# Kernel tuning notes

Measured on AMD Instinct MI355X. Metric: run time of the kernel, lower is better.

Reference implementation:

```python
import jax, jax.numpy as jnp
import numpy as np


def setup_inputs() -> dict:
    key = jax.random.key(0)
    k1, k2, k3 = jax.random.split(key, 3)
    B, K, NPC, D = 64, 1000, 256, 768
    querys = jax.random.normal(k1, (B, D), dtype=jnp.float32)
    data = jax.random.normal(k2, (K, NPC, D), dtype=jnp.float32)      # clustered doc embeddings
    centers = jax.random.normal(k3, (K, D), dtype=jnp.float32)        # cluster centroids
    clusted_idx = jnp.arange(K * NPC, dtype=jnp.int32).reshape(K, NPC)  # global doc id per slot
    return {
        'querys': querys,
        'data': data,
        'centers': centers,
        'clusted_idx': clusted_idx,
        'k': 16,
        'num_search': 10,
    }


def reference(querys, data, centers, clusted_idx, k, num_search):
    """Clustered (IVF-style) cosine top-k search.
    querys: (B,D); data: (K,NPC,D); centers: (K,D); clusted_idx: (K,NPC)
    returns ret_idx (B,k) int, ret_emb (B,k,D) float.
    dist_fn = -cos_sim, so argmin dist == argmax cosine.
    """
    B, D = querys.shape
    eps = jnp.float32(1e-12)
    qn = querys / jnp.maximum(jnp.linalg.norm(querys, axis=1, keepdims=True), eps)
    cn = centers / jnp.maximum(jnp.linalg.norm(centers, axis=1, keepdims=True), eps)

    # ---- first(): pick num_search closest clusters by cosine ----
    cos_c = qn @ cn.T                              # (B, K)
    _, c_idx = jax.lax.top_k(cos_c, num_search)    # (B, S) smallest -cos == largest cos

    # ---- second(): exact cosine search inside selected clusters ----
    cand = data[c_idx]                             # (B, S, NPC, D) gather
    cand_ids = clusted_idx[c_idx]                  # (B, S, NPC)
    cand_norm = jnp.maximum(jnp.linalg.norm(cand, axis=-1), eps)  # (B, S, NPC)
    cos = jnp.einsum('bd,bsnd->bsn', qn, cand) / cand_norm        # (B, S, NPC)

    # ---- merge: global top-k over all candidates ----
    cos_flat = cos.reshape(B, -1)                  # (B, S*NPC)
    _, top = jax.lax.top_k(cos_flat, k)            # (B, k)
    ret_idx = jnp.take_along_axis(cand_ids.reshape(B, -1), top, axis=1)            # (B, k)
    ret_emb = jnp.take_along_axis(cand.reshape(B, -1, D), top[..., None], axis=1)  # (B, k, D)
    return ret_idx, ret_emb
```

## Files before the change

kernel.cpp:

```cpp
#include <hip/hip_runtime.h>
#include <math.h>

#define BQ   64
#define KC   1000
#define NPC  256
#define DIM  768
#define TOPK 16
#define NS   10

#define NEG_INF (-__builtin_inff())

#define DOT12(acc, A, Bv) \
    acc = fmaf(A.x, Bv.x, acc); acc = fmaf(A.y, Bv.y, acc); \
    acc = fmaf(A.z, Bv.z, acc); acc = fmaf(A.w, Bv.w, acc);

__global__ void knorm_q(const float* __restrict__ q, float* __restrict__ qn) {
    int b = blockIdx.x, t = threadIdx.x;
    const float* row = q + b * DIM;
    float v0 = row[t], v1 = row[t + 256], v2 = row[t + 512];
    __shared__ float red[256];
    red[t] = v0 * v0 + v1 * v1 + v2 * v2;
    __syncthreads();
    for (int off = 128; off; off >>= 1) {
        if (t < off) red[t] += red[t + off];
        __syncthreads();
    }
    float scale = 1.0f / fmaxf(sqrtf(red[0]), 1e-12f);
    qn[b * DIM + t]       = v0 * scale;
    qn[b * DIM + t + 256] = v1 * scale;
    qn[b * DIM + t + 512] = v2 * scale;
}

__global__ void kcenter_scores(const float* __restrict__ qn,
                               const float* __restrict__ centers,
                               float* __restrict__ cosc) {
    int wave = threadIdx.x >> 6, lane = threadIdx.x & 63;
    int cblk = blockIdx.x >> 2, qg = blockIdx.x & 3;
    int k0 = cblk * 4 + wave;
    const float4* cp = (const float4*)(centers + (size_t)k0 * DIM);
    float4 c0 = cp[lane], c1 = cp[lane + 64], c2 = cp[lane + 128];
    float sq = 0.f;
    DOT12(sq, c0, c0); DOT12(sq, c1, c1); DOT12(sq, c2, c2);
    for (int off = 1; off < 64; off <<= 1) sq += __shfl_xor(sq, off);
    float inv = 1.0f / fmaxf(sqrtf(sq), 1e-12f);
    int b0 = qg * 16;
    for (int i = 0; i < 16; i += 4) {
        const float4* qa = (const float4*)(qn + (size_t)(b0 + i + 0) * DIM);
        const float4* qb = (const float4*)(qn + (size_t)(b0 + i + 1) * DIM);
        const float4* qc = (const float4*)(qn + (size_t)(b0 + i + 2) * DIM);
        const float4* qd = (const float4*)(qn + (size_t)(b0 + i + 3) * DIM);
        float4 a0 = qa[lane], a1 = qa[lane + 64], a2 = qa[lane + 128];
        float4 e0 = qb[lane], e1 = qb[lane + 64], e2 = qb[lane + 128];
        float4 f0 = qc[lane], f1 = qc[lane + 64], f2 = qc[lane + 128];
        float4 g0 = qd[lane], g1 = qd[lane + 64], g2 = qd[lane + 128];
        float dA = 0.f, dB = 0.f, dC = 0.f, dD = 0.f;
        DOT12(dA, a0, c0); DOT12(dA, a1, c1); DOT12(dA, a2, c2);
        DOT12(dB, e0, c0); DOT12(dB, e1, c1); DOT12(dB, e2, c2);
        DOT12(dC, f0, c0); DOT12(dC, f1, c1); DOT12(dC, f2, c2);
        DOT12(dD, g0, c0); DOT12(dD, g1, c1); DOT12(dD, g2, c2);
        for (int off = 1; off < 64; off <<= 1) {
            dA += __shfl_xor(dA, off);
            dB += __shfl_xor(dB, off);
            dC += __shfl_xor(dC, off);
            dD += __shfl_xor(dD, off);
        }
        if (lane == 0) {
            cosc[(b0 + i + 0) * KC + k0] = dA * inv;
            cosc[(b0 + i + 1) * KC + k0] = dB * inv;
            cosc[(b0 + i + 2) * KC + k0] = dC * inv;
            cosc[(b0 + i + 3) * KC + k0] = dD * inv;
        }
    }
}

__device__ __forceinline__ void wave_argmax(float& bv, int& bi) {
    for (int off = 1; off < 64; off <<= 1) {
        float v2 = __shfl_xor(bv, off);
        int   i2 = __shfl_xor(bi, off);
        if (v2 > bv || (v2 == bv && i2 < bi)) { bv = v2; bi = i2; }
    }
}

__global__ void ktop_clusters(const float* __restrict__ cosc, int* __restrict__ cidx) {
    int b = blockIdx.x, t = threadIdx.x;
    int wave = t >> 6, lane = t & 63;
    __shared__ float vals[KC];
    __shared__ float wrv[4];
    __shared__ int   wri[4];
    for (int i = t; i < KC; i += 256) vals[i] = cosc[b * KC + i];
    __syncthreads();
    for (int s = 0; s < NS; ++s) {
        float bv = NEG_INF; int bi = 0x7fffffff;
        for (int i = t; i < KC; i += 256) {
            float v = vals[i];
            if (v > bv) { bv = v; bi = i; }
        }
        wave_argmax(bv, bi);
        if (lane == 0) { wrv[wave] = bv; wri[wave] = bi; }
        __syncthreads();
        if (t == 0) {
            float fv = wrv[0]; int fi = wri[0];
            for (int w = 1; w < 4; ++w) {
                float v2 = wrv[w]; int i2 = wri[w];
                if (v2 > fv || (v2 == fv && i2 < fi)) { fv = v2; fi = i2; }
            }
            cidx[b * NS + s] = fi;
            vals[fi] = NEG_INF;
        }
        __syncthreads();
    }
}

__global__ void kcand(const float* __restrict__ qn, const float* __restrict__ data,
                      const int* __restrict__ cidx, float* __restrict__ cosall) {
    int blk = blockIdx.x;
    int pair = blk >> 2, sub = blk & 3;
    int b = pair / NS, s = pair - b * NS;
    int c = cidx[b * NS + s];
    int wave = threadIdx.x >> 6, lane = threadIdx.x & 63;
    const float4* qp = (const float4*)(qn + (size_t)b * DIM);
    float4 q0 = qp[lane], q1 = qp[lane + 64], q2 = qp[lane + 128];
    const float* base = data + (size_t)c * NPC * DIM;
    float* outp = cosall + (size_t)pair * NPC;
    int n0 = sub * 64 + wave * 16;
    for (int it = 0; it < 4; ++it) {
        int n = n0 + it * 4;
        const float4* dpa = (const float4*)(base + (size_t)(n + 0) * DIM);
        const float4* dpb = (const float4*)(base + (size_t)(n + 1) * DIM);
        const float4* dpc = (const float4*)(base + (size_t)(n + 2) * DIM);
        const float4* dpd = (const float4*)(base + (size_t)(n + 3) * DIM);
        float4 a0 = dpa[lane], a1 = dpa[lane + 64], a2 = dpa[lane + 128];
        float4 e0 = dpb[lane], e1 = dpb[lane + 64], e2 = dpb[lane + 128];
        float4 f0 = dpc[lane], f1 = dpc[lane + 64], f2 = dpc[lane + 128];
        float4 g0 = dpd[lane], g1 = dpd[lane + 64], g2 = dpd[lane + 128];
        float dotA = 0.f, sqA = 0.f, dotB = 0.f, sqB = 0.f;
        float dotC = 0.f, sqC = 0.f, dotD = 0.f, sqD = 0.f;
        DOT12(dotA, q0, a0); DOT12(dotA, q1, a1); DOT12(dotA, q2, a2);
        DOT12(sqA,  a0, a0); DOT12(sqA,  a1, a1); DOT12(sqA,  a2, a2);
        DOT12(dotB, q0, e0); DOT12(dotB, q1, e1); DOT12(dotB, q2, e2);
        DOT12(sqB,  e0, e0); DOT12(sqB,  e1, e1); DOT12(sqB,  e2, e2);
        DOT12(dotC, q0, f0); DOT12(dotC, q1, f1); DOT12(dotC, q2, f2);
        DOT12(sqC,  f0, f0); DOT12(sqC,  f1, f1); DOT12(sqC,  f2, f2);
        DOT12(dotD, q0, g0); DOT12(dotD, q1, g1); DOT12(dotD, q2, g2);
        DOT12(sqD,  g0, g0); DOT12(sqD,  g1, g1); DOT12(sqD,  g2, g2);
        for (int off = 1; off < 64; off <<= 1) {
            dotA += __shfl_xor(dotA, off); sqA += __shfl_xor(sqA, off);
            dotB += __shfl_xor(dotB, off); sqB += __shfl_xor(sqB, off);
            dotC += __shfl_xor(dotC, off); sqC += __shfl_xor(sqC, off);
            dotD += __shfl_xor(dotD, off); sqD += __shfl_xor(sqD, off);
        }
        if (lane == 0) {
            outp[n + 0] = dotA / fmaxf(sqrtf(sqA), 1e-12f);
            outp[n + 1] = dotB / fmaxf(sqrtf(sqB), 1e-12f);
            outp[n + 2] = dotC / fmaxf(sqrtf(sqC), 1e-12f);
            outp[n + 3] = dotD / fmaxf(sqrtf(sqD), 1e-12f);
        }
    }
}

__global__ void ktop_final(const float* __restrict__ cosall, const int* __restrict__ cidx,
                           const int* __restrict__ clusted, const float* __restrict__ data,
                           float* __restrict__ out) {
    int b = blockIdx.x, t = threadIdx.x;
    int wave = t >> 6, lane = t & 63;
    __shared__ float vals[NS * NPC];
    __shared__ float wrv[4];
    __shared__ int   wri[4];
    __shared__ int   docs[TOPK];
    for (int i = t; i < NS * NPC; i += 256) vals[i] = cosall[(size_t)b * (NS * NPC) + i];
    __syncthreads();
    for (int j = 0; j < TOPK; ++j) {
        float bv = NEG_INF; int bi = 0x7fffffff;
        for (int i = t; i < NS * NPC; i += 256) {
            float v = vals[i];
            if (v > bv) { bv = v; bi = i; }
        }
        wave_argmax(bv, bi);
        if (lane == 0) { wrv[wave] = bv; wri[wave] = bi; }
        __syncthreads();
        if (t == 0) {
            float fv = wrv[0]; int fi = wri[0];
            for (int w = 1; w < 4; ++w) {
                float v2 = wrv[w]; int i2 = wri[w];
                if (v2 > fv || (v2 == fv && i2 < fi)) { fv = v2; fi = i2; }
            }
            int s = fi >> 8, n = fi & (NPC - 1);
            int c = cidx[b * NS + s];
            int doc = c * NPC + n;
            docs[j] = doc;
            out[b * TOPK + j] = (float)clusted[doc];
            vals[fi] = NEG_INF;
        }
        __syncthreads();
    }
    float* emb = out + BQ * TOPK;
    for (int idx = t; idx < TOPK * (DIM / 4); idx += 256) {
        int j = idx / (DIM / 4), col = idx - j * (DIM / 4);
        int doc = docs[j];
        ((float4*)(emb + ((size_t)(b * TOPK + j)) * DIM))[col] =
            ((const float4*)(data + (size_t)doc * DIM))[col];
    }
}

extern "C" void kernel_launch(void* const* d_in, const int* in_sizes, int n_in,
                              void* d_out, int out_size, void* d_ws, size_t ws_size,
                              hipStream_t stream) {
    const float* querys  = (const float*)d_in[0];
    const float* data    = (const float*)d_in[1];
    const float* centers = (const float*)d_in[2];
    const int*   clusted = (const int*)d_in[3];
    float* out = (float*)d_out;

    float* ws     = (float*)d_ws;
    float* qn     = ws;
    float* cosc   = qn + BQ * DIM;
    int*   cidx   = (int*)(cosc + BQ * KC);
    float* cosall = (float*)(cidx + BQ * NS);

    knorm_q<<<BQ, 256, 0, stream>>>(querys, qn);
    kcenter_scores<<<KC, 256, 0, stream>>>(qn, centers, cosc);
    ktop_clusters<<<BQ, 256, 0, stream>>>(cosc, cidx);
    kcand<<<BQ * NS * 4, 256, 0, stream>>>(qn, data, cidx, cosall);
    ktop_final<<<BQ, 256, 0, stream>>>(cosall, cidx, clusted, data, out);
}
```

Baseline: 142.8 us.

## Invert candidate scoring to per-cluster blocks serving all queries that selected them

Builds an inverted list from each cluster to the (query, slot) pairs that selected it, using atomics in the cluster top-k kernel, with the counters zeroed in the query-norm kernel. The candidate kernel now launches one group of blocks per cluster. Each block loads the cluster's data rows once, computes their norms once, and loops over every query that picked that cluster. This removes redundant global reads of cluster data when several queries share a cluster, at the cost of launching blocks for unselected clusters (they exit early) and serialising work when a cluster is popular.

```diff
diff --git a/kernel.cpp b/kernel.cpp
--- a/kernel.cpp
+++ b/kernel.cpp
@@ -14,8 +14,10 @@
     acc = fmaf(A.x, Bv.x, acc); acc = fmaf(A.y, Bv.y, acc); \
     acc = fmaf(A.z, Bv.z, acc); acc = fmaf(A.w, Bv.w, acc);
 
-__global__ void knorm_q(const float* __restrict__ q, float* __restrict__ qn) {
+__global__ void knorm_q(const float* __restrict__ q, float* __restrict__ qn,
+                        int* __restrict__ cnt) {
     int b = blockIdx.x, t = threadIdx.x;
+    if (b < 4 && t < 250) cnt[b * 250 + t] = 0;
     const float* row = q + b * DIM;
     float v0 = row[t], v1 = row[t + 256], v2 = row[t + 512];
     __shared__ float red[256];
@@ -81,7 +83,8 @@
     }
 }
 
-__global__ void ktop_clusters(const float* __restrict__ cosc, int* __restrict__ cidx) {
+__global__ void ktop_clusters(const float* __restrict__ cosc, int* __restrict__ cidx,
+                              int* __restrict__ cnt, int* __restrict__ sel) {
     int b = blockIdx.x, t = threadIdx.x;
     int wave = t >> 6, lane = t & 63;
     __shared__ float vals[KC];
@@ -105,6 +108,8 @@
                 if (v2 > fv || (v2 == fv && i2 < fi)) { fv = v2; fi = i2; }
             }
             cidx[b * NS + s] = fi;
+            int pos = atomicAdd(&cnt[fi], 1);
+            sel[fi * 64 + pos] = b * NS + s;
             vals[fi] = NEG_INF;
         }
         __syncthreads();
@@ -112,16 +117,17 @@
 }
 
 __global__ void kcand(const float* __restrict__ qn, const float* __restrict__ data,
-                      const int* __restrict__ cidx, float* __restrict__ cosall) {
-    int blk = blockIdx.x;
-    int pair = blk >> 2, sub = blk & 3;
-    int b = pair / NS, s = pair - b * NS;
-    int c = cidx[b * NS + s];
-    int wave = threadIdx.x >> 6, lane = threadIdx.x & 63;
-    const float4* qp = (const float4*)(qn + (size_t)b * DIM);
-    float4 q0 = qp[lane], q1 = qp[lane + 64], q2 = qp[lane + 128];
+                      const int* __restrict__ cnt, const int* __restrict__ sel,
+                      float* __restrict__ cosall) {
+    int c = blockIdx.x >> 2, sub = blockIdx.x & 3;
+    int m = cnt[c];
+    if (m == 0) return;
+    int t = threadIdx.x;
+    __shared__ int slist[64];
+    if (t < m) slist[t] = sel[c * 64 + t];
+    __syncthreads();
+    int wave = t >> 6, lane = t & 63;
     const float* base = data + (size_t)c * NPC * DIM;
-    float* outp = cosall + (size_t)pair * NPC;
     int n0 = sub * 64 + wave * 16;
     for (int it = 0; it < 4; ++it) {
         int n = n0 + it * 4;
@@ -133,27 +139,40 @@
         float4 e0 = dpb[lane], e1 = dpb[lane + 64], e2 = dpb[lane + 128];
         float4 f0 = dpc[lane], f1 = dpc[lane + 64], f2 = dpc[lane + 128];
         float4 g0 = dpd[lane], g1 = dpd[lane + 64], g2 = dpd[lane + 128];
-        float dotA = 0.f, sqA = 0.f, dotB = 0.f, sqB = 0.f;
-        float dotC = 0.f, sqC = 0.f, dotD = 0.f, sqD = 0.f;
-        DOT12(dotA, q0, a0); DOT12(dotA, q1, a1); DOT12(dotA, q2, a2);
-        DOT12(sqA,  a0, a0); DOT12(sqA,  a1, a1); DOT12(sqA,  a2, a2);
-        DOT12(dotB, q0, e0); DOT12(dotB, q1, e1); DOT12(dotB, q2, e2);
-        DOT12(sqB,  e0, e0); DOT12(sqB,  e1, e1); DOT12(sqB,  e2, e2);
-        DOT12(dotC, q0, f0); DOT12(dotC, q1, f1); DOT12(dotC, q2, f2);
-        DOT12(sqC,  f0, f0); DOT12(sqC,  f1, f1); DOT12(sqC,  f2, f2);
-        DOT12(dotD, q0, g0); DOT12(dotD, q1, g1); DOT12(dotD, q2, g2);
-        DOT12(sqD,  g0, g0); DOT12(sqD,  g1, g1); DOT12(sqD,  g2, g2);
+        float sqA = 0.f, sqB = 0.f, sqC = 0.f, sqD = 0.f;
+        DOT12(sqA, a0, a0); DOT12(sqA, a1, a1); DOT12(sqA, a2, a2);
+        DOT12(sqB, e0, e0); DOT12(sqB, e1, e1); DOT12(sqB, e2, e2);
+        DOT12(sqC, f0, f0); DOT12(sqC, f1, f1); DOT12(sqC, f2, f2);
+        DOT12(sqD, g0, g0); DOT12(sqD, g1, g1); DOT12(sqD, g2, g2);
         for (int off = 1; off < 64; off <<= 1) {
-            dotA += __shfl_xor(dotA, off); sqA += __shfl_xor(sqA, off);
-            dotB += __shfl_xor(dotB, off); sqB += __shfl_xor(sqB, off);
-            dotC += __shfl_xor(dotC, off); sqC += __shfl_xor(sqC, off);
-            dotD += __shfl_xor(dotD, off); sqD += __shfl_xor(sqD, off);
-        }
-        if (lane == 0) {
-            outp[n + 0] = dotA / fmaxf(sqrtf(sqA), 1e-12f);
-            outp[n + 1] = dotB / fmaxf(sqrtf(sqB), 1e-12f);
-            outp[n + 2] = dotC / fmaxf(sqrtf(sqC), 1e-12f);
-            outp[n + 3] = dotD / fmaxf(sqrtf(sqD), 1e-12f);
+            sqA += __shfl_xor(sqA, off); sqB += __shfl_xor(sqB, off);
+            sqC += __shfl_xor(sqC, off); sqD += __shfl_xor(sqD, off);
+        }
+        float invA = 1.0f / fmaxf(sqrtf(sqA), 1e-12f);
+        float invB = 1.0f / fmaxf(sqrtf(sqB), 1e-12f);
+        float invC = 1.0f / fmaxf(sqrtf(sqC), 1e-12f);
+        float invD = 1.0f / fmaxf(sqrtf(sqD), 1e-12f);
+        for (int j = 0; j < m; ++j) {
+            int i = slist[j];
+            int b = i / NS;
+            const float4* qp = (const float4*)(qn + (size_t)b * DIM);
+            float4 q0 = qp[lane], q1 = qp[lane + 64], q2 = qp[lane + 128];
+            float dA = 0.f, dB = 0.f, dC = 0.f, dD = 0.f;
+            DOT12(dA, q0, a0); DOT12(dA, q1, a1); DOT12(dA, q2, a2);
+            DOT12(dB, q0, e0); DOT12(dB, q1, e1); DOT12(dB, q2, e2);
+            DOT12(dC, q0, f0); DOT12(dC, q1, f1); DOT12(dC, q2, f2);
+            DOT12(dD, q0, g0); DOT12(dD, q1, g1); DOT12(dD, q2, g2);
+            for (int off = 1; off < 64; off <<= 1) {
+                dA += __shfl_xor(dA, off); dB += __shfl_xor(dB, off);
+                dC += __shfl_xor(dC, off); dD += __shfl_xor(dD, off);
+            }
+            if (lane == 0) {
+                float* outp = cosall + (size_t)i * NPC + n;
+                outp[0] = dA * invA;
+                outp[1] = dB * invB;
+                outp[2] = dC * invC;
+                outp[3] = dD * invD;
+            }
         }
     }
 }
@@ -216,10 +235,12 @@
     float* cosc   = qn + BQ * DIM;
     int*   cidx   = (int*)(cosc + BQ * KC);
     float* cosall = (float*)(cidx + BQ * NS);
-
-    knorm_q<<<BQ, 256, 0, stream>>>(querys, qn);
+    int*   cnt    = (int*)(cosall + BQ * NS * NPC);
+    int*   sel    = cnt + KC;
+
+    knorm_q<<<BQ, 256, 0, stream>>>(querys, qn, cnt);
     kcenter_scores<<<KC, 256, 0, stream>>>(qn, centers, cosc);
-    ktop_clusters<<<BQ, 256, 0, stream>>>(cosc, cidx);
-    kcand<<<BQ * NS * 4, 256, 0, stream>>>(qn, data, cidx, cosall);
+    ktop_clusters<<<BQ, 256, 0, stream>>>(cosc, cidx, cnt, sel);
+    kcand<<<KC * 4, 256, 0, stream>>>(qn, data, cnt, sel, cosall);
     ktop_final<<<BQ, 256, 0, stream>>>(cosall, cidx, clusted, data, out);
 }
```

After: 143.1 us. No clear change (+0.2%).
